# Optimization experiments

Hardware: AMD Instinct MI355X
Metric: run time of the kernel (lower is better)

The kernel has to match this reference:

```python
import jax, jax.numpy as jnp
import numpy as np

N_NODES = 100000
D_SRC = 128
D_DST = 128
D_OUT = 256
N_EDGES = 600000


def setup_inputs() -> dict:
    key = jax.random.key(0)
    k1, k2, k3, k4, k5 = jax.random.split(key, 5)
    x_src = jax.random.normal(k1, (N_NODES, D_SRC), dtype=jnp.float32)
    x_dst = jax.random.normal(k2, (N_NODES, D_DST), dtype=jnp.float32)
    edge_index = jax.random.randint(k3, (2, N_EDGES), 0, N_NODES, dtype=jnp.int64)
    # Linear(in_src + in_dst, out): torch stores W as [out, in]
    fan_in = D_SRC + D_DST
    bound = 1.0 / np.sqrt(fan_in)
    W = jax.random.uniform(k4, (D_OUT, fan_in), minval=-bound, maxval=bound, dtype=jnp.float32)
    b = jax.random.uniform(k5, (D_OUT,), minval=-bound, maxval=bound, dtype=jnp.float32)
    return {"x_src": x_src, "x_dst": x_dst, "edge_index": edge_index, "W": W, "b": b}


def reference(x_src, x_dst, edge_index, W, b):
    src_idx, dst_idx = edge_index[0], edge_index[1]
    n_dst = x_dst.shape[0]
    x_j = x_src[src_idx]                                  # [E, D_SRC] gather
    summed = jax.ops.segment_sum(x_j, dst_idx, num_segments=n_dst)   # [N, D_SRC]
    count = jax.ops.segment_sum(jnp.ones((src_idx.shape[0],), dtype=x_src.dtype),
                                dst_idx, num_segments=n_dst)          # [N]
    agg = summed / jnp.maximum(count, 1.0)[:, None]        # scatter-mean
    h = jnp.concatenate([x_dst, agg], axis=-1)             # [N, D_DST+D_SRC]
    return jax.nn.relu(h @ W.T + b)                        # [N, D_OUT]
```

## Files before the change

kernel.cpp:

```cpp
#include <hip/hip_runtime.h>

#define N_NODES 100000
#define D_SRC 128
#define D_OUT 256
#define K_DIM 256
#define CAP 32
#define OVF_CAP 2048

typedef __attribute__((ext_vector_type(8))) short short8;
typedef __attribute__((ext_vector_type(4))) float float4v;
typedef __attribute__((ext_vector_type(4))) unsigned int uint4v;

__device__ inline unsigned short f2bf(float f) {
    unsigned int u = __float_as_uint(f);
    u += 0x7FFF + ((u >> 16) & 1);
    return (unsigned short)(u >> 16);
}
__device__ inline float bf_lo(unsigned int u) { return __uint_as_float(u << 16); }
__device__ inline float bf_hi(unsigned int u) { return __uint_as_float(u & 0xFFFF0000u); }

#define PREP_SRC_BLOCKS 12500
#define PREP_DST_BLOCKS 6250
#define PREP_W_BLOCKS   32
#define PREP_Z_BLOCKS   98
#define PREP_BLOCKS (PREP_SRC_BLOCKS + PREP_DST_BLOCKS + PREP_W_BLOCKS + PREP_Z_BLOCKS)

__global__ __launch_bounds__(256) void prep_kernel(
    const float* __restrict__ x_src,
    const float* __restrict__ x_dst,
    const float* __restrict__ W,
    unsigned short* __restrict__ xsb,
    unsigned short* __restrict__ xdsw,
    unsigned short* __restrict__ wsw,
    int* __restrict__ deg)
{
    int b = blockIdx.x;
    if (b < PREP_SRC_BLOCKS) {
        int i = b * 256 + threadIdx.x;
        float4 v = ((const float4*)x_src)[i];
        ushort4 o;
        o.x = f2bf(v.x); o.y = f2bf(v.y); o.z = f2bf(v.z); o.w = f2bf(v.w);
        ((ushort4*)xsb)[i] = o;
    } else if (b < PREP_SRC_BLOCKS + PREP_DST_BLOCKS) {
        int t = (b - PREP_SRC_BLOCKS) * 256 + threadIdx.x;
        int r = t >> 4;
        int g = t & 15;
        const float4* p = (const float4*)(x_dst + (size_t)r * 128 + g * 8);
        float4 v0 = p[0], v1 = p[1];
        union { unsigned short s[8]; short8 v; } pk;
        pk.s[0] = f2bf(v0.x); pk.s[1] = f2bf(v0.y);
        pk.s[2] = f2bf(v0.z); pk.s[3] = f2bf(v0.w);
        pk.s[4] = f2bf(v1.x); pk.s[5] = f2bf(v1.y);
        pk.s[6] = f2bf(v1.z); pk.s[7] = f2bf(v1.w);
        size_t gr = ((size_t)(r >> 4) * 4 + (g >> 2)) * 64 + (r & 15) + ((g & 3) << 4);
        ((short8*)xdsw)[gr] = pk.v;
    } else if (b < PREP_SRC_BLOCKS + PREP_DST_BLOCKS + PREP_W_BLOCKS) {
        int t = (b - PREP_SRC_BLOCKS - PREP_DST_BLOCKS) * 256 + threadIdx.x;
        int r = t >> 5;
        int g = t & 31;
        const float4* p = (const float4*)(W + (size_t)r * 256 + g * 8);
        float4 v0 = p[0], v1 = p[1];
        union { unsigned short s[8]; short8 v; } pk;
        pk.s[0] = f2bf(v0.x); pk.s[1] = f2bf(v0.y);
        pk.s[2] = f2bf(v0.z); pk.s[3] = f2bf(v0.w);
        pk.s[4] = f2bf(v1.x); pk.s[5] = f2bf(v1.y);
        pk.s[6] = f2bf(v1.z); pk.s[7] = f2bf(v1.w);
        size_t gr = ((size_t)(r >> 4) * 8 + (g >> 2)) * 64 + (r & 15) + ((g & 3) << 4);
        ((short8*)wsw)[gr] = pk.v;
    } else {
        int i = (b - PREP_SRC_BLOCKS - PREP_DST_BLOCKS - PREP_W_BLOCKS) * 256 + threadIdx.x;
        if (i < (N_NODES + 4) / 4)
            ((int4*)deg)[i] = make_int4(0, 0, 0, 0);
    }
}

__global__ __launch_bounds__(256) void bucket_kernel(
    const int* __restrict__ ei,
    int* __restrict__ deg,
    int* __restrict__ ovf_cnt,
    int* __restrict__ ovf,
    int* __restrict__ bucket,
    int n_edges)
{
    int e = blockIdx.x * 256 + threadIdx.x;
    if (e >= n_edges) return;
    int s = ei[e];
    int d = ei[n_edges + e];
    int pos = atomicAdd(deg + d, 1);
    if (pos < CAP) {
        bucket[(size_t)d * CAP + pos] = s;
    } else {
        int o = atomicAdd(ovf_cnt, 1);
        if (o < OVF_CAP) { ovf[2 * o] = s; ovf[2 * o + 1] = d; }
    }
}

#define G_ISSUE(U, V, B)                                                      \
    {                                                                         \
        int r_ = (B) + grp;                                                   \
        { bool v_ = r_ < n0; V[0] = v_; int s_ = __shfl(idx0, r_);            \
          s_ = v_ ? s_ : 0;                                                   \
          U[0] = *(const uint4v*)(xsb + (size_t)s_ * D_SRC + gcol * 8); }     \
        { bool v_ = r_ < n1; V[1] = v_; int s_ = __shfl(idx1, r_);            \
          s_ = v_ ? s_ : 0;                                                   \
          U[1] = *(const uint4v*)(xsb + (size_t)s_ * D_SRC + gcol * 8); }     \
        { bool v_ = r_ < n2; V[2] = v_; int s_ = __shfl(idx2, r_);            \
          s_ = v_ ? s_ : 0;                                                   \
          U[2] = *(const uint4v*)(xsb + (size_t)s_ * D_SRC + gcol * 8); }     \
        { bool v_ = r_ < n3; V[3] = v_; int s_ = __shfl(idx3, r_);            \
          s_ = v_ ? s_ : 0;                                                   \
          U[3] = *(const uint4v*)(xsb + (size_t)s_ * D_SRC + gcol * 8); }     \
    }

#define G_ACC1(ACC, W)                                                       \
    ACC[0] += bf_lo(W[0]); ACC[1] += bf_hi(W[0]);                            \
    ACC[2] += bf_lo(W[1]); ACC[3] += bf_hi(W[1]);                            \
    ACC[4] += bf_lo(W[2]); ACC[5] += bf_hi(W[2]);                            \
    ACC[6] += bf_lo(W[3]); ACC[7] += bf_hi(W[3]);

#define G_ACCUM(U, V)                                                        \
    if (V[0]) { G_ACC1(acc0, U[0]) }                                         \
    if (V[1]) { G_ACC1(acc1, U[1]) }                                         \
    if (V[2]) { G_ACC1(acc2, U[2]) }                                         \
    if (V[3]) { G_ACC1(acc3, U[3]) }

__global__ __launch_bounds__(256) void gather_kernel(
    const unsigned short* __restrict__ xsb,
    const int*   __restrict__ deg,
    const int*   __restrict__ bucket,
    const int*   __restrict__ ovf_cnt,
    const int*   __restrict__ ovf,
    unsigned int* __restrict__ aggsw)
{
    int wid  = threadIdx.x >> 6;
    int lane = threadIdx.x & 63;
    int nbase = (blockIdx.x * 4 + wid) * 4;
    if (nbase >= N_NODES) return;
    int grp  = lane >> 4;
    int gcol = lane & 15;

    int dl  = deg[nbase + (lane & 3)];
    int dt0 = __shfl(dl, 0), dt1 = __shfl(dl, 1);
    int dt2 = __shfl(dl, 2), dt3 = __shfl(dl, 3);
    int n0 = min(dt0, CAP), n1 = min(dt1, CAP);
    int n2 = min(dt2, CAP), n3 = min(dt3, CAP);

    int idx0 = bucket[(size_t)(nbase + 0) * CAP + (lane & 31)];
    int idx1 = bucket[(size_t)(nbase + 1) * CAP + (lane & 31)];
    int idx2 = bucket[(size_t)(nbase + 2) * CAP + (lane & 31)];
    int idx3 = bucket[(size_t)(nbase + 3) * CAP + (lane & 31)];

    float acc0[8] = {0,0,0,0,0,0,0,0}, acc1[8] = {0,0,0,0,0,0,0,0};
    float acc2[8] = {0,0,0,0,0,0,0,0}, acc3[8] = {0,0,0,0,0,0,0,0};

    int maxn = max(max(n0, n1), max(n2, n3));

    uint4v uA[4], uB[4];
    bool   vA[4], vB[4];
    if (maxn > 0) {
        G_ISSUE(uA, vA, 0)
        int b = 0;
        while (true) {
            if (b + 4 < maxn) { G_ISSUE(uB, vB, b + 4) }
            G_ACCUM(uA, vA)
            b += 4;
            if (b >= maxn) break;
            if (b + 4 < maxn) { G_ISSUE(uA, vA, b + 4) }
            G_ACCUM(uB, vB)
            b += 4;
            if (b >= maxn) break;
        }
    }

    if ((dt0 > CAP) | (dt1 > CAP) | (dt2 > CAP) | (dt3 > CAP)) {
        int oc = *ovf_cnt;
        if (oc > OVF_CAP) oc = OVF_CAP;
        for (int o = 0; o < oc; ++o) {
            int od  = ovf[2 * o + 1];
            int rel = od - nbase;
            if (rel >= 0 && rel < 4) {
                int s0 = ovf[2 * o];
                uint4v w = *(const uint4v*)(xsb + (size_t)s0 * D_SRC + gcol * 8);
                if (grp == 0) {
                    if      (rel == 0) { G_ACC1(acc0, w) }
                    else if (rel == 1) { G_ACC1(acc1, w) }
                    else if (rel == 2) { G_ACC1(acc2, w) }
                    else               { G_ACC1(acc3, w) }
                }
            }
        }
    }

    #pragma unroll
    for (int k = 0; k < 8; ++k) {
        acc0[k] += __shfl_xor(acc0[k], 16); acc0[k] += __shfl_xor(acc0[k], 32);
        acc1[k] += __shfl_xor(acc1[k], 16); acc1[k] += __shfl_xor(acc1[k], 32);
        acc2[k] += __shfl_xor(acc2[k], 16); acc2[k] += __shfl_xor(acc2[k], 32);
        acc3[k] += __shfl_xor(acc3[k], 16); acc3[k] += __shfl_xor(acc3[k], 32);
    }

    int dsel = dt0;
    dsel = (grp == 1) ? dt1 : dsel;
    dsel = (grp == 2) ? dt2 : dsel;
    dsel = (grp == 3) ? dt3 : dsel;
    float inv = 1.0f / (float)((dsel > 1) ? dsel : 1);

    float sum[8];
    #pragma unroll
    for (int k = 0; k < 8; ++k) {
        float v = acc0[k];
        v = (grp == 1) ? acc1[k] : v;
        v = (grp == 2) ? acc2[k] : v;
        v = (grp == 3) ? acc3[k] : v;
        sum[k] = v * inv;
    }

    uint4v o;
    o[0] = (unsigned)f2bf(sum[0]) | ((unsigned)f2bf(sum[1]) << 16);
    o[1] = (unsigned)f2bf(sum[2]) | ((unsigned)f2bf(sum[3]) << 16);
    o[2] = (unsigned)f2bf(sum[4]) | ((unsigned)f2bf(sum[5]) << 16);
    o[3] = (unsigned)f2bf(sum[6]) | ((unsigned)f2bf(sum[7]) << 16);

    int node = nbase + grp;
    size_t gr = ((size_t)(node >> 4) * 4 + (gcol >> 2)) * 64
              + (node & 15) + ((gcol & 3) << 4);
    ((uint4v*)aggsw)[gr] = o;
}

__global__ __launch_bounds__(256) void mfma_gemm_kernel(
    const short8* __restrict__ xdsw,
    const short8* __restrict__ aggsw,
    const short8* __restrict__ wsw,
    const float* __restrict__ bias,
    float*       __restrict__ out)
{
    __shared__ float eps[4][16][68];

    int wave = threadIdx.x >> 6;
    int lane = threadIdx.x & 63;
    int lrow = lane & 15;
    int kq   = lane >> 4;
    int mb   = blockIdx.x;
    int m0   = mb * 64;
    int n0   = wave * 64;

    bool mok[4];
    #pragma unroll
    for (int mf = 0; mf < 4; ++mf) mok[mf] = (m0 + mf * 16) < N_NODES;

    const short8* Ax = xdsw  + (size_t)mb * 1024 + lane;
    const short8* Ag = aggsw + (size_t)mb * 1024 + lane;
    const short8* Bw = wsw   + (size_t)wave * 2048 + lane;

    float4v acc[4][4];
    #pragma unroll
    for (int i = 0; i < 4; ++i)
        #pragma unroll
        for (int j = 0; j < 4; ++j)
            acc[i][j] = (float4v){0.f, 0.f, 0.f, 0.f};

    const short8 zfrag = (short8){0,0,0,0,0,0,0,0};
    short8 a[2][4], b[2][4];

    #pragma unroll
    for (int mf = 0; mf < 4; ++mf)
        a[0][mf] = mok[mf] ? Ax[mf * 256] : zfrag;
    #pragma unroll
    for (int nf = 0; nf < 4; ++nf)
        b[0][nf] = Bw[nf * 512];

    #pragma unroll
    for (int kc = 0; kc < 8; ++kc) {
        const int cur = kc & 1, nxt = cur ^ 1;
        if (kc < 7) {
            const int k1 = kc + 1;
            const short8* A = (k1 < 4) ? Ax : Ag;
            const int kk = (k1 < 4) ? k1 : (k1 - 4);
            #pragma unroll
            for (int mf = 0; mf < 4; ++mf)
                a[nxt][mf] = mok[mf] ? A[mf * 256 + kk * 64] : zfrag;
            #pragma unroll
            for (int nf = 0; nf < 4; ++nf)
                b[nxt][nf] = Bw[nf * 512 + k1 * 64];
        }
        #pragma unroll
        for (int mf = 0; mf < 4; ++mf)
            #pragma unroll
            for (int nf = 0; nf < 4; ++nf)
                acc[mf][nf] = __builtin_amdgcn_mfma_f32_16x16x32_bf16(
                    a[cur][mf], b[cur][nf], acc[mf][nf], 0, 0, 0);
    }

    float bv[4];
    #pragma unroll
    for (int nf = 0; nf < 4; ++nf)
        bv[nf] = bias[n0 + nf * 16 + lrow];

    int srow   = lane >> 4;
    int schunk = lane & 15;

    #pragma unroll
    for (int mf = 0; mf < 4; ++mf) {
        if (!mok[mf]) continue;
        #pragma unroll
        for (int nf = 0; nf < 4; ++nf)
            #pragma unroll
            for (int r = 0; r < 4; ++r)
                eps[wave][kq * 4 + r][nf * 16 + lrow] =
                    fmaxf(acc[mf][nf][r] + bv[nf], 0.f);
        asm volatile("s_waitcnt lgkmcnt(0)" ::: "memory");
        #pragma unroll
        for (int c = 0; c < 4; ++c) {
            int row  = c * 4 + srow;
            float4v v = *(const float4v*)&eps[wave][row][schunk * 4];
            int grow = m0 + mf * 16 + row;
            __builtin_nontemporal_store(v,
                (float4v*)(out + (size_t)grow * D_OUT + n0 + schunk * 4));
        }
        asm volatile("s_waitcnt lgkmcnt(0)" ::: "memory");
    }
}

extern "C" void kernel_launch(void* const* d_in, const int* in_sizes, int n_in,
                              void* d_out, int out_size, void* d_ws, size_t ws_size,
                              hipStream_t stream) {
    const float* x_src = (const float*)d_in[0];
    const float* x_dst = (const float*)d_in[1];
    const int*   ei    = (const int*)d_in[2];
    const float* W     = (const float*)d_in[3];
    const float* bias  = (const float*)d_in[4];
    float* out = (float*)d_out;

    int n_edges = in_sizes[2] / 2;

    int* deg     = (int*)d_ws;
    int* ovf_cnt = deg + N_NODES;
    int* ovf     = ovf_cnt + 4;
    unsigned short* wsw   = (unsigned short*)(ovf + OVF_CAP * 2);
    unsigned short* aggsw = wsw + (size_t)D_OUT * K_DIM;
    unsigned short* xdsw  = aggsw + (size_t)(N_NODES / 16) * 4 * 64 * 8;

    int* bucket = (int*)d_out;
    unsigned short* xsb = (unsigned short*)(bucket + (size_t)N_NODES * CAP);

    prep_kernel<<<PREP_BLOCKS, 256, 0, stream>>>(
        x_src, x_dst, W, xsb, xdsw, wsw, deg);

    bucket_kernel<<<(n_edges + 255) / 256, 256, 0, stream>>>(
        ei, deg, ovf_cnt, ovf, bucket, n_edges);

    gather_kernel<<<(N_NODES + 15) / 16, 256, 0, stream>>>(
        xsb, deg, bucket, ovf_cnt, ovf, (unsigned int*)aggsw);

    mfma_gemm_kernel<<<(N_NODES + 63) / 64, 256, 0, stream>>>(
        (const short8*)xdsw, (const short8*)aggsw, (const short8*)wsw, bias, out);
}
```

Before: 289.8 us.

## Fuse neighbor gather-mean into MFMA GEMM through shared-memory staging

Merges the gather/scatter-mean kernel into the GEMM kernel. Each block computes the aggregated bf16 neighbor means for its 64 rows and writes them into a 16 KB LDS tile in MFMA fragment layout. The GEMM then reads the second half of K from that tile instead of from a global aggsw buffer. This removes the global write and re-read of the aggregate array and one kernel launch. Because output is now written while other blocks still read the buckets, the bucket and bf16 source buffers move from the output buffer into the workspace. The cost is that gather work is serialized within each wave before the MFMA loop starts, so fewer independent gather waves are in flight.

```diff
diff --git a/kernel.cpp b/kernel.cpp
--- a/kernel.cpp
+++ b/kernel.cpp
@@ -124,133 +124,138 @@
     if (V[2]) { G_ACC1(acc2, U[2]) }                                         \
     if (V[3]) { G_ACC1(acc3, U[3]) }
 
-__global__ __launch_bounds__(256) void gather_kernel(
+__global__ __launch_bounds__(256) void fused_gather_gemm_kernel(
     const unsigned short* __restrict__ xsb,
     const int*   __restrict__ deg,
     const int*   __restrict__ bucket,
     const int*   __restrict__ ovf_cnt,
     const int*   __restrict__ ovf,
-    unsigned int* __restrict__ aggsw)
-{
-    int wid  = threadIdx.x >> 6;
-    int lane = threadIdx.x & 63;
-    int nbase = (blockIdx.x * 4 + wid) * 4;
-    if (nbase >= N_NODES) return;
-    int grp  = lane >> 4;
-    int gcol = lane & 15;
-
-    int dl  = deg[nbase + (lane & 3)];
-    int dt0 = __shfl(dl, 0), dt1 = __shfl(dl, 1);
-    int dt2 = __shfl(dl, 2), dt3 = __shfl(dl, 3);
-    int n0 = min(dt0, CAP), n1 = min(dt1, CAP);
-    int n2 = min(dt2, CAP), n3 = min(dt3, CAP);
-
-    int idx0 = bucket[(size_t)(nbase + 0) * CAP + (lane & 31)];
-    int idx1 = bucket[(size_t)(nbase + 1) * CAP + (lane & 31)];
-    int idx2 = bucket[(size_t)(nbase + 2) * CAP + (lane & 31)];
-    int idx3 = bucket[(size_t)(nbase + 3) * CAP + (lane & 31)];
-
-    float acc0[8] = {0,0,0,0,0,0,0,0}, acc1[8] = {0,0,0,0,0,0,0,0};
-    float acc2[8] = {0,0,0,0,0,0,0,0}, acc3[8] = {0,0,0,0,0,0,0,0};
-
-    int maxn = max(max(n0, n1), max(n2, n3));
-
-    uint4v uA[4], uB[4];
-    bool   vA[4], vB[4];
-    if (maxn > 0) {
-        G_ISSUE(uA, vA, 0)
-        int b = 0;
-        while (true) {
-            if (b + 4 < maxn) { G_ISSUE(uB, vB, b + 4) }
-            G_ACCUM(uA, vA)
-            b += 4;
-            if (b >= maxn) break;
-            if (b + 4 < maxn) { G_ISSUE(uA, vA, b + 4) }
-            G_ACCUM(uB, vB)
-            b += 4;
-            if (b >= maxn) break;
-        }
-    }
-
-    if ((dt0 > CAP) | (dt1 > CAP) | (dt2 > CAP) | (dt3 > CAP)) {
-        int oc = *ovf_cnt;
-        if (oc > OVF_CAP) oc = OVF_CAP;
-        for (int o = 0; o < oc; ++o) {
-            int od  = ovf[2 * o + 1];
-            int rel = od - nbase;
-            if (rel >= 0 && rel < 4) {
-                int s0 = ovf[2 * o];
-                uint4v w = *(const uint4v*)(xsb + (size_t)s0 * D_SRC + gcol * 8);
-                if (grp == 0) {
-                    if      (rel == 0) { G_ACC1(acc0, w) }
-                    else if (rel == 1) { G_ACC1(acc1, w) }
-                    else if (rel == 2) { G_ACC1(acc2, w) }
-                    else               { G_ACC1(acc3, w) }
-                }
-            }
-        }
-    }
-
-    #pragma unroll
-    for (int k = 0; k < 8; ++k) {
-        acc0[k] += __shfl_xor(acc0[k], 16); acc0[k] += __shfl_xor(acc0[k], 32);
-        acc1[k] += __shfl_xor(acc1[k], 16); acc1[k] += __shfl_xor(acc1[k], 32);
-        acc2[k] += __shfl_xor(acc2[k], 16); acc2[k] += __shfl_xor(acc2[k], 32);
-        acc3[k] += __shfl_xor(acc3[k], 16); acc3[k] += __shfl_xor(acc3[k], 32);
-    }
-
-    int dsel = dt0;
-    dsel = (grp == 1) ? dt1 : dsel;
-    dsel = (grp == 2) ? dt2 : dsel;
-    dsel = (grp == 3) ? dt3 : dsel;
-    float inv = 1.0f / (float)((dsel > 1) ? dsel : 1);
-
-    float sum[8];
-    #pragma unroll
-    for (int k = 0; k < 8; ++k) {
-        float v = acc0[k];
-        v = (grp == 1) ? acc1[k] : v;
-        v = (grp == 2) ? acc2[k] : v;
-        v = (grp == 3) ? acc3[k] : v;
-        sum[k] = v * inv;
-    }
-
-    uint4v o;
-    o[0] = (unsigned)f2bf(sum[0]) | ((unsigned)f2bf(sum[1]) << 16);
-    o[1] = (unsigned)f2bf(sum[2]) | ((unsigned)f2bf(sum[3]) << 16);
-    o[2] = (unsigned)f2bf(sum[4]) | ((unsigned)f2bf(sum[5]) << 16);
-    o[3] = (unsigned)f2bf(sum[6]) | ((unsigned)f2bf(sum[7]) << 16);
-
-    int node = nbase + grp;
-    size_t gr = ((size_t)(node >> 4) * 4 + (gcol >> 2)) * 64
-              + (node & 15) + ((gcol & 3) << 4);
-    ((uint4v*)aggsw)[gr] = o;
-}
-
-__global__ __launch_bounds__(256) void mfma_gemm_kernel(
     const short8* __restrict__ xdsw,
-    const short8* __restrict__ aggsw,
     const short8* __restrict__ wsw,
     const float* __restrict__ bias,
     float*       __restrict__ out)
 {
+    __shared__ uint4v lds_agg[1024];
     __shared__ float eps[4][16][68];
 
-    int wave = threadIdx.x >> 6;
-    int lane = threadIdx.x & 63;
-    int lrow = lane & 15;
-    int kq   = lane >> 4;
-    int mb   = blockIdx.x;
-    int m0   = mb * 64;
-    int n0   = wave * 64;
+    const int wave = threadIdx.x >> 6;
+    const int lane = threadIdx.x & 63;
+    const int mb   = blockIdx.x;
+    const int m0   = mb * 64;
+    const int grp  = lane >> 4;
+    const int gcol = lane & 15;
+    const int lrow = lane & 15;
+    const int kq   = lane >> 4;
+    const int nc0  = wave * 64;
 
     bool mok[4];
     #pragma unroll
     for (int mf = 0; mf < 4; ++mf) mok[mf] = (m0 + mf * 16) < N_NODES;
 
-    const short8* Ax = xdsw  + (size_t)mb * 1024 + lane;
-    const short8* Ag = aggsw + (size_t)mb * 1024 + lane;
-    const short8* Bw = wsw   + (size_t)wave * 2048 + lane;
+    const short8* Ax = xdsw + (size_t)mb * 1024 + lane;
+    const short8* Bw = wsw  + (size_t)wave * 2048 + lane;
+
+    const short8 zfrag = (short8){0,0,0,0,0,0,0,0};
+    short8 a[2][4], b[2][4];
+    #pragma unroll
+    for (int mf = 0; mf < 4; ++mf)
+        a[0][mf] = mok[mf] ? Ax[mf * 256] : zfrag;
+    #pragma unroll
+    for (int nf = 0; nf < 4; ++nf)
+        b[0][nf] = Bw[nf * 512];
+
+    for (int q = 0; q < 4; ++q) {
+        int nbase = m0 + wave * 16 + q * 4;
+
+        int dl = 0;
+        { int nidx = nbase + (lane & 3);
+          if (nidx < N_NODES) dl = deg[nidx]; }
+        int dt0 = __shfl(dl, 0), dt1 = __shfl(dl, 1);
+        int dt2 = __shfl(dl, 2), dt3 = __shfl(dl, 3);
+        int n0 = min(dt0, CAP), n1 = min(dt1, CAP);
+        int n2 = min(dt2, CAP), n3 = min(dt3, CAP);
+
+        int idx0 = bucket[(size_t)(nbase + 0) * CAP + (lane & 31)];
+        int idx1 = bucket[(size_t)(nbase + 1) * CAP + (lane & 31)];
+        int idx2 = bucket[(size_t)(nbase + 2) * CAP + (lane & 31)];
+        int idx3 = bucket[(size_t)(nbase + 3) * CAP + (lane & 31)];
+
+        float acc0[8] = {0,0,0,0,0,0,0,0}, acc1[8] = {0,0,0,0,0,0,0,0};
+        float acc2[8] = {0,0,0,0,0,0,0,0}, acc3[8] = {0,0,0,0,0,0,0,0};
+
+        int maxn = max(max(n0, n1), max(n2, n3));
+
+        uint4v uA[4], uB[4];
+        bool   vA[4], vB[4];
+        if (maxn > 0) {
+            G_ISSUE(uA, vA, 0)
+            int bb = 0;
+            while (true) {
+                if (bb + 4 < maxn) { G_ISSUE(uB, vB, bb + 4) }
+                G_ACCUM(uA, vA)
+                bb += 4;
+                if (bb >= maxn) break;
+                if (bb + 4 < maxn) { G_ISSUE(uA, vA, bb + 4) }
+                G_ACCUM(uB, vB)
+                bb += 4;
+                if (bb >= maxn) break;
+            }
+        }
+
+        if ((dt0 > CAP) | (dt1 > CAP) | (dt2 > CAP) | (dt3 > CAP)) {
+            int oc = *ovf_cnt;
+            if (oc > OVF_CAP) oc = OVF_CAP;
+            for (int o = 0; o < oc; ++o) {
+                int od  = ovf[2 * o + 1];
+                int rel = od - nbase;
+                if (rel >= 0 && rel < 4) {
+                    int s0 = ovf[2 * o];
+                    uint4v w = *(const uint4v*)(xsb + (size_t)s0 * D_SRC + gcol * 8);
+                    if (grp == 0) {
+                        if      (rel == 0) { G_ACC1(acc0, w) }
+                        else if (rel == 1) { G_ACC1(acc1, w) }
+                        else if (rel == 2) { G_ACC1(acc2, w) }
+                        else               { G_ACC1(acc3, w) }
+                    }
+                }
+            }
+        }
+
+        #pragma unroll
+        for (int k = 0; k < 8; ++k) {
+            acc0[k] += __shfl_xor(acc0[k], 16); acc0[k] += __shfl_xor(acc0[k], 32);
+            acc1[k] += __shfl_xor(acc1[k], 16); acc1[k] += __shfl_xor(acc1[k], 32);
+            acc2[k] += __shfl_xor(acc2[k], 16); acc2[k] += __shfl_xor(acc2[k], 32);
+            acc3[k] += __shfl_xor(acc3[k], 16); acc3[k] += __shfl_xor(acc3[k], 32);
+        }
+
+        int dsel = dt0;
+        dsel = (grp == 1) ? dt1 : dsel;
+        dsel = (grp == 2) ? dt2 : dsel;
+        dsel = (grp == 3) ? dt3 : dsel;
+        float inv = 1.0f / (float)((dsel > 1) ? dsel : 1);
+
+        float sum[8];
+        #pragma unroll
+        for (int k = 0; k < 8; ++k) {
+            float v = acc0[k];
+            v = (grp == 1) ? acc1[k] : v;
+            v = (grp == 2) ? acc2[k] : v;
+            v = (grp == 3) ? acc3[k] : v;
+            sum[k] = v * inv;
+        }
+
+        uint4v o;
+        o[0] = (unsigned)f2bf(sum[0]) | ((unsigned)f2bf(sum[1]) << 16);
+        o[1] = (unsigned)f2bf(sum[2]) | ((unsigned)f2bf(sum[3]) << 16);
+        o[2] = (unsigned)f2bf(sum[4]) | ((unsigned)f2bf(sum[5]) << 16);
+        o[3] = (unsigned)f2bf(sum[6]) | ((unsigned)f2bf(sum[7]) << 16);
+
+        int gr = (wave * 4 + (gcol >> 2)) * 64 + (q * 4 + grp) + ((gcol & 3) << 4);
+        lds_agg[gr] = o;
+    }
+
+    __syncthreads();
 
     float4v acc[4][4];
     #pragma unroll
@@ -258,27 +263,22 @@
         #pragma unroll
         for (int j = 0; j < 4; ++j)
             acc[i][j] = (float4v){0.f, 0.f, 0.f, 0.f};
-
-    const short8 zfrag = (short8){0,0,0,0,0,0,0,0};
-    short8 a[2][4], b[2][4];
-
-    #pragma unroll
-    for (int mf = 0; mf < 4; ++mf)
-        a[0][mf] = mok[mf] ? Ax[mf * 256] : zfrag;
-    #pragma unroll
-    for (int nf = 0; nf < 4; ++nf)
-        b[0][nf] = Bw[nf * 512];
 
     #pragma unroll
     for (int kc = 0; kc < 8; ++kc) {
         const int cur = kc & 1, nxt = cur ^ 1;
         if (kc < 7) {
             const int k1 = kc + 1;
-            const short8* A = (k1 < 4) ? Ax : Ag;
-            const int kk = (k1 < 4) ? k1 : (k1 - 4);
-            #pragma unroll
-            for (int mf = 0; mf < 4; ++mf)
-                a[nxt][mf] = mok[mf] ? A[mf * 256 + kk * 64] : zfrag;
+            if (k1 < 4) {
+                #pragma unroll
+                for (int mf = 0; mf < 4; ++mf)
+                    a[nxt][mf] = mok[mf] ? Ax[mf * 256 + k1 * 64] : zfrag;
+            } else {
+                const int kk = k1 - 4;
+                #pragma unroll
+                for (int mf = 0; mf < 4; ++mf)
+                    a[nxt][mf] = *(const short8*)&lds_agg[(mf * 4 + kk) * 64 + lane];
+            }
             #pragma unroll
             for (int nf = 0; nf < 4; ++nf)
                 b[nxt][nf] = Bw[nf * 512 + k1 * 64];
@@ -294,7 +294,7 @@
     float bv[4];
     #pragma unroll
     for (int nf = 0; nf < 4; ++nf)
-        bv[nf] = bias[n0 + nf * 16 + lrow];
+        bv[nf] = bias[nc0 + nf * 16 + lrow];
 
     int srow   = lane >> 4;
     int schunk = lane & 15;
@@ -315,7 +315,7 @@
             float4v v = *(const float4v*)&eps[wave][row][schunk * 4];
             int grow = m0 + mf * 16 + row;
             __builtin_nontemporal_store(v,
-                (float4v*)(out + (size_t)grow * D_OUT + n0 + schunk * 4));
+                (float4v*)(out + (size_t)grow * D_OUT + nc0 + schunk * 4));
         }
         asm volatile("s_waitcnt lgkmcnt(0)" ::: "memory");
     }
@@ -336,11 +336,9 @@
     int* deg     = (int*)d_ws;
     int* ovf_cnt = deg + N_NODES;
     int* ovf     = ovf_cnt + 4;
-    unsigned short* wsw   = (unsigned short*)(ovf + OVF_CAP * 2);
-    unsigned short* aggsw = wsw + (size_t)D_OUT * K_DIM;
-    unsigned short* xdsw  = aggsw + (size_t)(N_NODES / 16) * 4 * 64 * 8;
-
-    int* bucket = (int*)d_out;
+    unsigned short* wsw  = (unsigned short*)(ovf + OVF_CAP * 2);
+    unsigned short* xdsw = wsw + (size_t)D_OUT * K_DIM;
+    int* bucket = (int*)(xdsw + (size_t)(N_NODES / 16) * 4 * 64 * 8);
     unsigned short* xsb = (unsigned short*)(bucket + (size_t)N_NODES * CAP);
 
     prep_kernel<<<PREP_BLOCKS, 256, 0, stream>>>(
@@ -349,9 +347,7 @@
     bucket_kernel<<<(n_edges + 255) / 256, 256, 0, stream>>>(
         ei, deg, ovf_cnt, ovf, bucket, n_edges);
 
-    gather_kernel<<<(N_NODES + 15) / 16, 256, 0, stream>>>(
-        xsb, deg, bucket, ovf_cnt, ovf, (unsigned int*)aggsw);
-
-    mfma_gemm_kernel<<<(N_NODES + 63) / 64, 256, 0, stream>>>(
-        (const short8*)xdsw, (const short8*)aggsw, (const short8*)wsw, bias, out);
-}
+    fused_gather_gemm_kernel<<<(N_NODES + 63) / 64, 256, 0, stream>>>(
+        xsb, deg, bucket, ovf_cnt, ovf,
+        (const short8*)xdsw, (const short8*)wsw, bias, out);
+}
```

Measured after the change: 302.1 us. 4.3% more time.

## Gather 8 nodes per wave and bucket 2 edges per thread

Applied to the files above, without the earlier changes.

The gather kernel now has each wave handle two groups of four destination nodes. This doubles the number of independent row loads in flight per iteration, to hide the latency of random gathers from the source features. The bucket kernel reads source and destination indices as int2 and processes two edges per thread, which halves the thread count. The cost is much higher register use in the gather kernel (twice the accumulators and load buffers), which may lower occupancy.

```diff
diff --git a/kernel.cpp b/kernel.cpp
--- a/kernel.cpp
+++ b/kernel.cpp
@@ -82,32 +82,51 @@
     int* __restrict__ bucket,
     int n_edges)
 {
-    int e = blockIdx.x * 256 + threadIdx.x;
-    if (e >= n_edges) return;
-    int s = ei[e];
-    int d = ei[n_edges + e];
-    int pos = atomicAdd(deg + d, 1);
-    if (pos < CAP) {
-        bucket[(size_t)d * CAP + pos] = s;
-    } else {
-        int o = atomicAdd(ovf_cnt, 1);
-        if (o < OVF_CAP) { ovf[2 * o] = s; ovf[2 * o + 1] = d; }
-    }
-}
-
-#define G_ISSUE(U, V, B)                                                      \
+    int t = blockIdx.x * 256 + threadIdx.x;
+    int e0 = 2 * t;
+    if (e0 + 1 < n_edges) {
+        int2 s2 = ((const int2*)ei)[t];
+        int2 d2 = ((const int2*)(ei + n_edges))[t];
+        int pos0 = atomicAdd(deg + d2.x, 1);
+        if (pos0 < CAP) {
+            bucket[(size_t)d2.x * CAP + pos0] = s2.x;
+        } else {
+            int o = atomicAdd(ovf_cnt, 1);
+            if (o < OVF_CAP) { ovf[2 * o] = s2.x; ovf[2 * o + 1] = d2.x; }
+        }
+        int pos1 = atomicAdd(deg + d2.y, 1);
+        if (pos1 < CAP) {
+            bucket[(size_t)d2.y * CAP + pos1] = s2.y;
+        } else {
+            int o = atomicAdd(ovf_cnt, 1);
+            if (o < OVF_CAP) { ovf[2 * o] = s2.y; ovf[2 * o + 1] = d2.y; }
+        }
+    } else if (e0 < n_edges) {
+        int s = ei[e0];
+        int d = ei[n_edges + e0];
+        int pos = atomicAdd(deg + d, 1);
+        if (pos < CAP) {
+            bucket[(size_t)d * CAP + pos] = s;
+        } else {
+            int o = atomicAdd(ovf_cnt, 1);
+            if (o < OVF_CAP) { ovf[2 * o] = s; ovf[2 * o + 1] = d; }
+        }
+    }
+}
+
+#define G_ISSUE8(U, V, B, I0, I1, I2, I3, N0, N1, N2, N3)                     \
     {                                                                         \
         int r_ = (B) + grp;                                                   \
-        { bool v_ = r_ < n0; V[0] = v_; int s_ = __shfl(idx0, r_);            \
+        { bool v_ = r_ < N0; V[0] = v_; int s_ = __shfl(I0, r_);              \
           s_ = v_ ? s_ : 0;                                                   \
           U[0] = *(const uint4v*)(xsb + (size_t)s_ * D_SRC + gcol * 8); }     \
-        { bool v_ = r_ < n1; V[1] = v_; int s_ = __shfl(idx1, r_);            \
+        { bool v_ = r_ < N1; V[1] = v_; int s_ = __shfl(I1, r_);              \
           s_ = v_ ? s_ : 0;                                                   \
           U[1] = *(const uint4v*)(xsb + (size_t)s_ * D_SRC + gcol * 8); }     \
-        { bool v_ = r_ < n2; V[2] = v_; int s_ = __shfl(idx2, r_);            \
+        { bool v_ = r_ < N2; V[2] = v_; int s_ = __shfl(I2, r_);              \
           s_ = v_ ? s_ : 0;                                                   \
           U[2] = *(const uint4v*)(xsb + (size_t)s_ * D_SRC + gcol * 8); }     \
-        { bool v_ = r_ < n3; V[3] = v_; int s_ = __shfl(idx3, r_);            \
+        { bool v_ = r_ < N3; V[3] = v_; int s_ = __shfl(I3, r_);              \
           s_ = v_ ? s_ : 0;                                                   \
           U[3] = *(const uint4v*)(xsb + (size_t)s_ * D_SRC + gcol * 8); }     \
     }
@@ -118,11 +137,11 @@
     ACC[4] += bf_lo(W[2]); ACC[5] += bf_hi(W[2]);                            \
     ACC[6] += bf_lo(W[3]); ACC[7] += bf_hi(W[3]);
 
-#define G_ACCUM(U, V)                                                        \
-    if (V[0]) { G_ACC1(acc0, U[0]) }                                         \
-    if (V[1]) { G_ACC1(acc1, U[1]) }                                         \
-    if (V[2]) { G_ACC1(acc2, U[2]) }                                         \
-    if (V[3]) { G_ACC1(acc3, U[3]) }
+#define G_ACCUM8(U, V, A0, A1, A2, A3)                                       \
+    if (V[0]) { G_ACC1(A0, U[0]) }                                           \
+    if (V[1]) { G_ACC1(A1, U[1]) }                                           \
+    if (V[2]) { G_ACC1(A2, U[2]) }                                           \
+    if (V[3]) { G_ACC1(A3, U[3]) }
 
 __global__ __launch_bounds__(256) void gather_kernel(
     const unsigned short* __restrict__ xsb,
@@ -134,58 +153,82 @@
 {
     int wid  = threadIdx.x >> 6;
     int lane = threadIdx.x & 63;
-    int nbase = (blockIdx.x * 4 + wid) * 4;
-    if (nbase >= N_NODES) return;
+    int wbase = (blockIdx.x * 4 + wid) * 8;
     int grp  = lane >> 4;
     int gcol = lane & 15;
 
-    int dl  = deg[nbase + (lane & 3)];
-    int dt0 = __shfl(dl, 0), dt1 = __shfl(dl, 1);
-    int dt2 = __shfl(dl, 2), dt3 = __shfl(dl, 3);
-    int n0 = min(dt0, CAP), n1 = min(dt1, CAP);
-    int n2 = min(dt2, CAP), n3 = min(dt3, CAP);
-
-    int idx0 = bucket[(size_t)(nbase + 0) * CAP + (lane & 31)];
-    int idx1 = bucket[(size_t)(nbase + 1) * CAP + (lane & 31)];
-    int idx2 = bucket[(size_t)(nbase + 2) * CAP + (lane & 31)];
-    int idx3 = bucket[(size_t)(nbase + 3) * CAP + (lane & 31)];
-
-    float acc0[8] = {0,0,0,0,0,0,0,0}, acc1[8] = {0,0,0,0,0,0,0,0};
-    float acc2[8] = {0,0,0,0,0,0,0,0}, acc3[8] = {0,0,0,0,0,0,0,0};
-
-    int maxn = max(max(n0, n1), max(n2, n3));
-
-    uint4v uA[4], uB[4];
-    bool   vA[4], vB[4];
+    int dl = deg[wbase + (lane & 7)];
+    int dtA0 = __shfl(dl, 0), dtA1 = __shfl(dl, 1);
+    int dtA2 = __shfl(dl, 2), dtA3 = __shfl(dl, 3);
+    int dtB0 = __shfl(dl, 4), dtB1 = __shfl(dl, 5);
+    int dtB2 = __shfl(dl, 6), dtB3 = __shfl(dl, 7);
+    int nA0 = min(dtA0, CAP), nA1 = min(dtA1, CAP);
+    int nA2 = min(dtA2, CAP), nA3 = min(dtA3, CAP);
+    int nB0 = min(dtB0, CAP), nB1 = min(dtB1, CAP);
+    int nB2 = min(dtB2, CAP), nB3 = min(dtB3, CAP);
+
+    int iA0 = bucket[(size_t)(wbase + 0) * CAP + (lane & 31)];
+    int iA1 = bucket[(size_t)(wbase + 1) * CAP + (lane & 31)];
+    int iA2 = bucket[(size_t)(wbase + 2) * CAP + (lane & 31)];
+    int iA3 = bucket[(size_t)(wbase + 3) * CAP + (lane & 31)];
+    int iB0 = bucket[(size_t)(wbase + 4) * CAP + (lane & 31)];
+    int iB1 = bucket[(size_t)(wbase + 5) * CAP + (lane & 31)];
+    int iB2 = bucket[(size_t)(wbase + 6) * CAP + (lane & 31)];
+    int iB3 = bucket[(size_t)(wbase + 7) * CAP + (lane & 31)];
+
+    float accA0[8] = {0,0,0,0,0,0,0,0}, accA1[8] = {0,0,0,0,0,0,0,0};
+    float accA2[8] = {0,0,0,0,0,0,0,0}, accA3[8] = {0,0,0,0,0,0,0,0};
+    float accB0[8] = {0,0,0,0,0,0,0,0}, accB1[8] = {0,0,0,0,0,0,0,0};
+    float accB2[8] = {0,0,0,0,0,0,0,0}, accB3[8] = {0,0,0,0,0,0,0,0};
+
+    int maxn = max(max(max(nA0, nA1), max(nA2, nA3)),
+                   max(max(nB0, nB1), max(nB2, nB3)));
+
+    uint4v uAa[4], uAb[4], uBa[4], uBb[4];
+    bool   vAa[4], vAb[4], vBa[4], vBb[4];
     if (maxn > 0) {
-        G_ISSUE(uA, vA, 0)
-        int b = 0;
+        G_ISSUE8(uAa, vAa, 0, iA0, iA1, iA2, iA3, nA0, nA1, nA2, nA3)
+        G_ISSUE8(uBa, vBa, 0, iB0, iB1, iB2, iB3, nB0, nB1, nB2, nB3)
+        int bb = 0;
         while (true) {
-            if (b + 4 < maxn) { G_ISSUE(uB, vB, b + 4) }
-            G_ACCUM(uA, vA)
-            b += 4;
-            if (b >= maxn) break;
-            if (b + 4 < maxn) { G_ISSUE(uA, vA, b + 4) }
-            G_ACCUM(uB, vB)
-            b += 4;
-            if (b >= maxn) break;
-        }
-    }
-
-    if ((dt0 > CAP) | (dt1 > CAP) | (dt2 > CAP) | (dt3 > CAP)) {
+            if (bb + 4 < maxn) {
+                G_ISSUE8(uAb, vAb, bb + 4, iA0, iA1, iA2, iA3, nA0, nA1, nA2, nA3)
+                G_ISSUE8(uBb, vBb, bb + 4, iB0, iB1, iB2, iB3, nB0, nB1, nB2, nB3)
+            }
+            G_ACCUM8(uAa, vAa, accA0, accA1, accA2, accA3)
+            G_ACCUM8(uBa, vBa, accB0, accB1, accB2, accB3)
+            bb += 4;
+            if (bb >= maxn) break;
+            if (bb + 4 < maxn) {
+                G_ISSUE8(uAa, vAa, bb + 4, iA0, iA1, iA2, iA3, nA0, nA1, nA2, nA3)
+                G_ISSUE8(uBa, vBa, bb + 4, iB0, iB1, iB2, iB3, nB0, nB1, nB2, nB3)
+            }
+            G_ACCUM8(uAb, vAb, accA0, accA1, accA2, accA3)
+            G_ACCUM8(uBb, vBb, accB0, accB1, accB2, accB3)
+            bb += 4;
+            if (bb >= maxn) break;
+        }
+    }
+
+    if ((dtA0 > CAP) | (dtA1 > CAP) | (dtA2 > CAP) | (dtA3 > CAP) |
+        (dtB0 > CAP) | (dtB1 > CAP) | (dtB2 > CAP) | (dtB3 > CAP)) {
         int oc = *ovf_cnt;
         if (oc > OVF_CAP) oc = OVF_CAP;
         for (int o = 0; o < oc; ++o) {
             int od  = ovf[2 * o + 1];
-            int rel = od - nbase;
-            if (rel >= 0 && rel < 4) {
+            int rel = od - wbase;
+            if (rel >= 0 && rel < 8) {
                 int s0 = ovf[2 * o];
                 uint4v w = *(const uint4v*)(xsb + (size_t)s0 * D_SRC + gcol * 8);
                 if (grp == 0) {
-                    if      (rel == 0) { G_ACC1(acc0, w) }
-                    else if (rel == 1) { G_ACC1(acc1, w) }
-                    else if (rel == 2) { G_ACC1(acc2, w) }
-                    else               { G_ACC1(acc3, w) }
+                    if      (rel == 0) { G_ACC1(accA0, w) }
+                    else if (rel == 1) { G_ACC1(accA1, w) }
+                    else if (rel == 2) { G_ACC1(accA2, w) }
+                    else if (rel == 3) { G_ACC1(accA3, w) }
+                    else if (rel == 4) { G_ACC1(accB0, w) }
+                    else if (rel == 5) { G_ACC1(accB1, w) }
+                    else if (rel == 6) { G_ACC1(accB2, w) }
+                    else               { G_ACC1(accB3, w) }
                 }
             }
         }
@@ -193,38 +236,66 @@
 
     #pragma unroll
     for (int k = 0; k < 8; ++k) {
-        acc0[k] += __shfl_xor(acc0[k], 16); acc0[k] += __shfl_xor(acc0[k], 32);
-        acc1[k] += __shfl_xor(acc1[k], 16); acc1[k] += __shfl_xor(acc1[k], 32);
-        acc2[k] += __shfl_xor(acc2[k], 16); acc2[k] += __shfl_xor(acc2[k], 32);
-        acc3[k] += __shfl_xor(acc3[k], 16); acc3[k] += __shfl_xor(acc3[k], 32);
-    }
-
-    int dsel = dt0;
-    dsel = (grp == 1) ? dt1 : dsel;
-    dsel = (grp == 2) ? dt2 : dsel;
-    dsel = (grp == 3) ? dt3 : dsel;
-    float inv = 1.0f / (float)((dsel > 1) ? dsel : 1);
-
-    float sum[8];
-    #pragma unroll
-    for (int k = 0; k < 8; ++k) {
-        float v = acc0[k];
-        v = (grp == 1) ? acc1[k] : v;
-        v = (grp == 2) ? acc2[k] : v;
-        v = (grp == 3) ? acc3[k] : v;
-        sum[k] = v * inv;
-    }
-
-    uint4v o;
-    o[0] = (unsigned)f2bf(sum[0]) | ((unsigned)f2bf(sum[1]) << 16);
-    o[1] = (unsigned)f2bf(sum[2]) | ((unsigned)f2bf(sum[3]) << 16);
-    o[2] = (unsigned)f2bf(sum[4]) | ((unsigned)f2bf(sum[5]) << 16);
-    o[3] = (unsigned)f2bf(sum[6]) | ((unsigned)f2bf(sum[7]) << 16);
-
-    int node = nbase + grp;
-    size_t gr = ((size_t)(node >> 4) * 4 + (gcol >> 2)) * 64
-              + (node & 15) + ((gcol & 3) << 4);
-    ((uint4v*)aggsw)[gr] = o;
+        accA0[k] += __shfl_xor(accA0[k], 16); accA0[k] += __shfl_xor(accA0[k], 32);
+        accA1[k] += __shfl_xor(accA1[k], 16); accA1[k] += __shfl_xor(accA1[k], 32);
+        accA2[k] += __shfl_xor(accA2[k], 16); accA2[k] += __shfl_xor(accA2[k], 32);
+        accA3[k] += __shfl_xor(accA3[k], 16); accA3[k] += __shfl_xor(accA3[k], 32);
+        accB0[k] += __shfl_xor(accB0[k], 16); accB0[k] += __shfl_xor(accB0[k], 32);
+        accB1[k] += __shfl_xor(accB1[k], 16); accB1[k] += __shfl_xor(accB1[k], 32);
+        accB2[k] += __shfl_xor(accB2[k], 16); accB2[k] += __shfl_xor(accB2[k], 32);
+        accB3[k] += __shfl_xor(accB3[k], 16); accB3[k] += __shfl_xor(accB3[k], 32);
+    }
+
+    {
+        int dsel = dtA0;
+        dsel = (grp == 1) ? dtA1 : dsel;
+        dsel = (grp == 2) ? dtA2 : dsel;
+        dsel = (grp == 3) ? dtA3 : dsel;
+        float inv = 1.0f / (float)((dsel > 1) ? dsel : 1);
+        float sum[8];
+        #pragma unroll
+        for (int k = 0; k < 8; ++k) {
+            float v = accA0[k];
+            v = (grp == 1) ? accA1[k] : v;
+            v = (grp == 2) ? accA2[k] : v;
+            v = (grp == 3) ? accA3[k] : v;
+            sum[k] = v * inv;
+        }
+        uint4v o;
+        o[0] = (unsigned)f2bf(sum[0]) | ((unsigned)f2bf(sum[1]) << 16);
+        o[1] = (unsigned)f2bf(sum[2]) | ((unsigned)f2bf(sum[3]) << 16);
+        o[2] = (unsigned)f2bf(sum[4]) | ((unsigned)f2bf(sum[5]) << 16);
+        o[3] = (unsigned)f2bf(sum[6]) | ((unsigned)f2bf(sum[7]) << 16);
+        int node = wbase + grp;
+        size_t gr = ((size_t)(node >> 4) * 4 + (gcol >> 2)) * 64
+                  + (node & 15) + ((gcol & 3) << 4);
+        ((uint4v*)aggsw)[gr] = o;
+    }
+    {
+        int dsel = dtB0;
+        dsel = (grp == 1) ? dtB1 : dsel;
+        dsel = (grp == 2) ? dtB2 : dsel;
+        dsel = (grp == 3) ? dtB3 : dsel;
+        float inv = 1.0f / (float)((dsel > 1) ? dsel : 1);
+        float sum[8];
+        #pragma unroll
+        for (int k = 0; k < 8; ++k) {
+            float v = accB0[k];
+            v = (grp == 1) ? accB1[k] : v;
+            v = (grp == 2) ? accB2[k] : v;
+            v = (grp == 3) ? accB3[k] : v;
+            sum[k] = v * inv;
+        }
+        uint4v o;
+        o[0] = (unsigned)f2bf(sum[0]) | ((unsigned)f2bf(sum[1]) << 16);
+        o[1] = (unsigned)f2bf(sum[2]) | ((unsigned)f2bf(sum[3]) << 16);
+        o[2] = (unsigned)f2bf(sum[4]) | ((unsigned)f2bf(sum[5]) << 16);
+        o[3] = (unsigned)f2bf(sum[6]) | ((unsigned)f2bf(sum[7]) << 16);
+        int node = wbase + 4 + grp;
+        size_t gr = ((size_t)(node >> 4) * 4 + (gcol >> 2)) * 64
+                  + (node & 15) + ((gcol & 3) << 4);
+        ((uint4v*)aggsw)[gr] = o;
+    }
 }
 
 __global__ __launch_bounds__(256) void mfma_gemm_kernel(
@@ -346,10 +417,11 @@
     prep_kernel<<<PREP_BLOCKS, 256, 0, stream>>>(
         x_src, x_dst, W, xsb, xdsw, wsw, deg);
 
-    bucket_kernel<<<(n_edges + 255) / 256, 256, 0, stream>>>(
+    int n_pairs = (n_edges + 1) / 2;
+    bucket_kernel<<<(n_pairs + 255) / 256, 256, 0, stream>>>(
         ei, deg, ovf_cnt, ovf, bucket, n_edges);
 
-    gather_kernel<<<(N_NODES + 15) / 16, 256, 0, stream>>>(
+    gather_kernel<<<(N_NODES + 31) / 32, 256, 0, stream>>>(
         xsb, deg, bucket, ovf_cnt, ovf, (unsigned int*)aggsw);
 
     mfma_gemm_kernel<<<(N_NODES + 63) / 64, 256, 0, stream>>>(
```

Result: no change. 286.2 us (-1.2%).
